# Kernel tuning notes

Measured on AMD Instinct MI355X. Metric: run time of the kernel, lower is better.

The kernel has to match this reference:

```python
import jax, jax.numpy as jnp
import numpy as np

B, S, D, NF = 4, 8192, 1024, 256

def setup_inputs() -> dict:
    key = jax.random.key(0)
    k1, k2, k3, k4 = jax.random.split(key, 4)
    x = jax.random.normal(k1, (B, S, D), dtype=jnp.float32)
    W_in = jax.random.normal(k2, (2 * NF, D), dtype=jnp.float32) * 0.02
    W_out = jax.random.normal(k3, (D, 2 * NF), dtype=jnp.float32) * 0.02
    log_decay = jnp.linspace(-3.0, -0.001, NF).astype(jnp.float32)
    frequencies = jax.random.normal(k4, (NF,), dtype=jnp.float32)
    return {"x": x, "W_in": W_in, "W_out": W_out,
            "log_decay": log_decay, "frequencies": frequencies}

def reference(x, W_in, W_out, log_decay, frequencies):
    b, s, d = x.shape
    nf = log_decay.shape[0]
    dt = jnp.float32(1.0)
    # system matrices
    decay = jax.nn.sigmoid(log_decay)                      # [nf]
    omega = frequencies * 0.1 * dt
    rot = jax.lax.complex(jnp.cos(omega), jnp.sin(omega))  # [nf] complex
    A = decay * rot                                        # [nf] complex
    # input projection -> complex signal u
    spectral = jnp.einsum('bsd,fd->bsf', x, W_in)          # [b,s,2nf]
    u = jax.lax.complex(spectral[..., :nf], spectral[..., nf:])  # [b,s,nf]
    # kernel: powers[t] = A^t via cumprod (matches torch numerics), times rot
    ones = jnp.ones((1, nf), dtype=A.dtype)
    A_rep = jnp.broadcast_to(A[None, :], (s - 1, nf))
    powers = jnp.cumprod(jnp.concatenate([ones, A_rep], axis=0), axis=0)  # [s,nf]
    kernel = powers * rot[None, :]                         # [s,nf]
    # FFT long convolution (zero-pad to 2s for linear conv)
    n_fft = 2 * s
    U_f = jnp.fft.fft(u, n=n_fft, axis=1)                  # [b,2s,nf]
    K_f = jnp.fft.fft(kernel, n=n_fft, axis=0)             # [2s,nf]
    y = jnp.fft.ifft(U_f * K_f[None, :, :], axis=1)[:, :s, :]  # [b,s,nf]
    feats = jnp.concatenate([y.real, y.imag], axis=-1)     # [b,s,2nf]
    return jnp.einsum('bsf,df->bsd', feats, W_out)         # [b,s,d]
```

## Files before the change

### kernel.cpp

```cpp
#include <hip/hip_runtime.h>
#include <math.h>
#include <stdint.h>

#define PB 4
#define PS 8192
#define PD 1024
#define PNF 256
#define PF2 512
#define PM 32768

#define CHUNK_L 32
#define WARM_W 32
#define NCHUNK (PS / CHUNK_L)

typedef __bf16 bf16x8 __attribute__((ext_vector_type(8)));
typedef float f32x4 __attribute__((ext_vector_type(4)));

__device__ __forceinline__ unsigned short f2bf(float f) {
  uint32_t b = __float_as_uint(f);
  b += 0x7FFFu + ((b >> 16) & 1u);
  return (unsigned short)(b >> 16);
}
__device__ __forceinline__ float bf2f(unsigned short u) {
  return __uint_as_float(((uint32_t)u) << 16);
}

__device__ __forceinline__ void gload16(const void* g, void* l) {
  __builtin_amdgcn_global_load_lds(
      (const __attribute__((address_space(1))) void*)g,
      (__attribute__((address_space(3))) void*)l, 16, 0, 0);
}

__global__ __launch_bounds__(256) void cvt_f32_bf16(
    const float* __restrict__ in, unsigned short* __restrict__ out, int n8) {
  int i = blockIdx.x * 256 + threadIdx.x;
  const int stride = gridDim.x * 256;
  for (; i < n8; i += stride) {
    const float4* p = (const float4*)(in + (size_t)i * 8);
    float4 a = p[0], b = p[1];
    float v[8] = {a.x, a.y, a.z, a.w, b.x, b.y, b.z, b.w};
    union { unsigned short u[8]; uint4 q; } o;
#pragma unroll
    for (int j = 0; j < 8; ++j) o.u[j] = f2bf(v[j]);
    *(uint4*)(out + (size_t)i * 8) = o.q;
  }
}

template <bool STORE_BF16>
__global__ __launch_bounds__(256, 2) void gemm_nt_mfma(
    const unsigned short* __restrict__ A, const unsigned short* __restrict__ Bt,
    void* __restrict__ Cv, int M, int N, int K) {
  __shared__ __align__(16) unsigned short As[128 * 32];
  __shared__ __align__(16) unsigned short Bs[128 * 32];
  const int tid = threadIdx.x;
  const int lane = tid & 63;
  const int w = tid >> 6;
  const int bm = blockIdx.y * 128;
  const int bn = blockIdx.x * 128;
  const int wm = (w >> 1) * 64;
  const int wn = (w & 1) * 64;

  const int lr = tid >> 2;
  const int lc = (tid & 3) * 8;
  const unsigned short* Ap = A + (size_t)(bm + lr) * K + lc;
  const unsigned short* Bp = Bt + (size_t)(bn + lr) * K + lc;
  char* AsB0 = (char*)As + (size_t)(w * 64) * 16;
  char* AsB1 = (char*)As + (size_t)(256 + w * 64) * 16;
  char* BsB0 = (char*)Bs + (size_t)(w * 64) * 16;
  char* BsB1 = (char*)Bs + (size_t)(256 + w * 64) * 16;

  const int fr = lane & 15;
  const int fk = (lane >> 4) * 8;

  f32x4 acc[4][4] = {};

  const int nk = K >> 5;
  for (int kk = 0; kk < nk; ++kk) {
    __syncthreads();
    gload16(Ap, AsB0);
    gload16(Ap + (size_t)64 * K, AsB1);
    gload16(Bp, BsB0);
    gload16(Bp + (size_t)64 * K, BsB1);
    Ap += 32; Bp += 32;
    __syncthreads();

    bf16x8 af[4], bfr[4];
#pragma unroll
    for (int mi = 0; mi < 4; ++mi)
      af[mi] = *(const bf16x8*)&As[(wm + mi * 16 + fr) * 32 + fk];
#pragma unroll
    for (int ni = 0; ni < 4; ++ni)
      bfr[ni] = *(const bf16x8*)&Bs[(wn + ni * 16 + fr) * 32 + fk];
#pragma unroll
    for (int mi = 0; mi < 4; ++mi)
#pragma unroll
      for (int ni = 0; ni < 4; ++ni)
        acc[mi][ni] = __builtin_amdgcn_mfma_f32_16x16x32_bf16(
            af[mi], bfr[ni], acc[mi][ni], 0, 0, 0);
  }

  const int orow0 = bm + wm + (lane >> 4) * 4;
  const int ocol0 = bn + wn + (lane & 15);
  if (STORE_BF16) {
    unsigned short* C = (unsigned short*)Cv;
#pragma unroll
    for (int mi = 0; mi < 4; ++mi)
#pragma unroll
      for (int ni = 0; ni < 4; ++ni) {
        const int col = ocol0 + ni * 16;
#pragma unroll
        for (int j = 0; j < 4; ++j) {
          const int row = orow0 + mi * 16 + j;
          C[(size_t)row * N + col] = f2bf(acc[mi][ni][j]);
        }
      }
  } else {
    float* C = (float*)Cv;
#pragma unroll
    for (int mi = 0; mi < 4; ++mi)
#pragma unroll
      for (int ni = 0; ni < 4; ++ni) {
        const int col = ocol0 + ni * 16;
#pragma unroll
        for (int j = 0; j < 4; ++j) {
          const int row = orow0 + mi * 16 + j;
          C[(size_t)row * N + col] = acc[mi][ni][j];
        }
      }
  }
}

__global__ __launch_bounds__(256) void scan_fused(
    const unsigned short* __restrict__ sp, const float* __restrict__ log_decay,
    const float* __restrict__ freq, unsigned short* __restrict__ feats) {
  const int tid = threadIdx.x;
  const int half = tid >> 7;
  const int fp = tid & 127;
  const int f0 = fp * 2;
  const int c = blockIdx.x * 2 + half;
  const int b = blockIdx.y;

  float Ar[2], Ai[2], rc_[2], rs_[2], hr[2] = {0.f, 0.f}, hi[2] = {0.f, 0.f};
#pragma unroll
  for (int k = 0; k < 2; ++k) {
    const float decay = 1.f / (1.f + expf(-log_decay[f0 + k]));
    const float om = freq[f0 + k] * 0.1f;
    rc_[k] = cosf(om); rs_[k] = sinf(om);
    Ar[k] = decay * rc_[k]; Ai[k] = decay * rs_[k];
  }

  const int t0 = c * CHUNK_L;
  int tw = t0 - WARM_W; if (tw < 0) tw = 0;
  const uint32_t* base = (const uint32_t*)(sp + (size_t)b * PS * PF2);
  uint32_t* ob = (uint32_t*)(feats + (size_t)b * PS * PF2);
  const int pr_off = f0 >> 1;
  const int pi_off = (PNF + f0) >> 1;

  for (int t = tw; t < t0; ++t) {
    const size_t rowu = (size_t)t * (PF2 / 2);
    uint32_t pr = base[rowu + pr_off];
    uint32_t pi = base[rowu + pi_off];
    float ur[2] = {bf2f((unsigned short)(pr & 0xffff)), bf2f((unsigned short)(pr >> 16))};
    float ui[2] = {bf2f((unsigned short)(pi & 0xffff)), bf2f((unsigned short)(pi >> 16))};
#pragma unroll
    for (int k = 0; k < 2; ++k) {
      float nr = fmaf(Ar[k], hr[k], fmaf(-Ai[k], hi[k], ur[k]));
      float ni = fmaf(Ar[k], hi[k], fmaf(Ai[k], hr[k], ui[k]));
      hr[k] = nr; hi[k] = ni;
    }
  }
  for (int t = t0; t < t0 + CHUNK_L; ++t) {
    const size_t rowu = (size_t)t * (PF2 / 2);
    uint32_t pr = base[rowu + pr_off];
    uint32_t pi = base[rowu + pi_off];
    float ur[2] = {bf2f((unsigned short)(pr & 0xffff)), bf2f((unsigned short)(pr >> 16))};
    float ui[2] = {bf2f((unsigned short)(pi & 0xffff)), bf2f((unsigned short)(pi >> 16))};
    uint32_t wr = 0, wi = 0;
#pragma unroll
    for (int k = 0; k < 2; ++k) {
      float nr = fmaf(Ar[k], hr[k], fmaf(-Ai[k], hi[k], ur[k]));
      float ni = fmaf(Ar[k], hi[k], fmaf(Ai[k], hr[k], ui[k]));
      hr[k] = nr; hi[k] = ni;
      const float yr = fmaf(rc_[k], hr[k], -rs_[k] * hi[k]);
      const float yi = fmaf(rc_[k], hi[k],  rs_[k] * hr[k]);
      wr |= (uint32_t)f2bf(yr) << (16 * k);
      wi |= (uint32_t)f2bf(yi) << (16 * k);
    }
    ob[rowu + pr_off] = wr;
    ob[rowu + pi_off] = wi;
  }
}

extern "C" void kernel_launch(void* const* d_in, const int* in_sizes, int n_in,
                              void* d_out, int out_size, void* d_ws, size_t ws_size,
                              hipStream_t stream) {
  const float* x         = (const float*)d_in[0];
  const float* W_in      = (const float*)d_in[1];
  const float* W_out     = (const float*)d_in[2];
  const float* log_decay = (const float*)d_in[3];
  const float* freq      = (const float*)d_in[4];
  float* out = (float*)d_out;

  unsigned short* xbf   = (unsigned short*)d_ws;
  unsigned short* wibf  = xbf + (size_t)PM * PD;
  unsigned short* wobf  = wibf + (size_t)PF2 * PD;
  unsigned short* spbf  = wobf + (size_t)PD * PF2;
  unsigned short* feats = xbf;

  cvt_f32_bf16<<<2048, 256, 0, stream>>>(x, xbf, PM * PD / 8);
  cvt_f32_bf16<<<256, 256, 0, stream>>>(W_in, wibf, PF2 * PD / 8);
  cvt_f32_bf16<<<256, 256, 0, stream>>>(W_out, wobf, PD * PF2 / 8);

  gemm_nt_mfma<true><<<dim3(PF2 / 128, PM / 128), 256, 0, stream>>>(
      xbf, wibf, spbf, PM, PF2, PD);

  scan_fused<<<dim3(NCHUNK / 2, PB), 256, 0, stream>>>(spbf, log_decay, freq, feats);

  gemm_nt_mfma<false><<<dim3(PD / 128, PM / 128), 256, 0, stream>>>(
      feats, wobf, out, PM, PD, PF2);
}
```

Measured before the change: 364.0 us.

## Replace GEMM with 256x256-tile 8-phase pipelined MFMA kernel

Replaces the simple 128x128 single-buffered GEMM with a 512-thread 256x256-tile kernel that double-buffers 64-wide K slices in 128 KB of dynamic LDS. It interleaves global-to-LDS loads with MFMA phases using explicit waitcnt, barriers and setprio, and applies an XOR swizzle to reduce LDS bank conflicts. It also pads the workspace buffers. The aim is to hide memory latency and raise MFMA utilisation. The cost is heavy LDS use (one block per CU) and fragile hand-tuned wait counts.

```diff
diff --git a/kernel.cpp b/kernel.cpp
--- a/kernel.cpp
+++ b/kernel.cpp
@@ -24,7 +24,6 @@
 __device__ __forceinline__ float bf2f(unsigned short u) {
   return __uint_as_float(((uint32_t)u) << 16);
 }
-
 __device__ __forceinline__ void gload16(const void* g, void* l) {
   __builtin_amdgcn_global_load_lds(
       (const __attribute__((address_space(1))) void*)g,
@@ -47,87 +46,116 @@
 }
 
 template <bool STORE_BF16>
-__global__ __launch_bounds__(256, 2) void gemm_nt_mfma(
-    const unsigned short* __restrict__ A, const unsigned short* __restrict__ Bt,
+__global__ __launch_bounds__(512, 2) void gemm_nt_8phase(
+    const unsigned short* __restrict__ Ag, const unsigned short* __restrict__ Bg,
     void* __restrict__ Cv, int M, int N, int K) {
-  __shared__ __align__(16) unsigned short As[128 * 32];
-  __shared__ __align__(16) unsigned short Bs[128 * 32];
+  extern __shared__ char smem[];
+  char* AtC = smem;
+  char* BtC = smem + 65536;
   const int tid = threadIdx.x;
   const int lane = tid & 63;
   const int w = tid >> 6;
-  const int bm = blockIdx.y * 128;
-  const int bn = blockIdx.x * 128;
-  const int wm = (w >> 1) * 64;
-  const int wn = (w & 1) * 64;
-
-  const int lr = tid >> 2;
-  const int lc = (tid & 3) * 8;
-  const unsigned short* Ap = A + (size_t)(bm + lr) * K + lc;
-  const unsigned short* Bp = Bt + (size_t)(bn + lr) * K + lc;
-  char* AsB0 = (char*)As + (size_t)(w * 64) * 16;
-  char* AsB1 = (char*)As + (size_t)(256 + w * 64) * 16;
-  char* BsB0 = (char*)Bs + (size_t)(w * 64) * 16;
-  char* BsB1 = (char*)Bs + (size_t)(256 + w * 64) * 16;
-
+  const int wr = w >> 2, wc = w & 3;
+  const int bm = blockIdx.y * 256, bn = blockIdx.x * 256;
   const int fr = lane & 15;
-  const int fk = (lane >> 4) * 8;
-
-  f32x4 acc[4][4] = {};
-
-  const int nk = K >> 5;
-  for (int kk = 0; kk < nk; ++kk) {
-    __syncthreads();
-    gload16(Ap, AsB0);
-    gload16(Ap + (size_t)64 * K, AsB1);
-    gload16(Bp, BsB0);
-    gload16(Bp + (size_t)64 * K, BsB1);
-    Ap += 32; Bp += 32;
-    __syncthreads();
-
-    bf16x8 af[4], bfr[4];
-#pragma unroll
-    for (int mi = 0; mi < 4; ++mi)
-      af[mi] = *(const bf16x8*)&As[(wm + mi * 16 + fr) * 32 + fk];
-#pragma unroll
-    for (int ni = 0; ni < 4; ++ni)
-      bfr[ni] = *(const bf16x8*)&Bs[(wn + ni * 16 + fr) * 32 + fk];
-#pragma unroll
-    for (int mi = 0; mi < 4; ++mi)
-#pragma unroll
-      for (int ni = 0; ni < 4; ++ni)
-        acc[mi][ni] = __builtin_amdgcn_mfma_f32_16x16x32_bf16(
-            af[mi], bfr[ni], acc[mi][ni], 0, 0, 0);
-  }
-
-  const int orow0 = bm + wm + (lane >> 4) * 4;
-  const int ocol0 = bn + wn + (lane & 15);
-  if (STORE_BF16) {
-    unsigned short* C = (unsigned short*)Cv;
-#pragma unroll
-    for (int mi = 0; mi < 4; ++mi)
-#pragma unroll
-      for (int ni = 0; ni < 4; ++ni) {
-        const int col = ocol0 + ni * 16;
-#pragma unroll
-        for (int j = 0; j < 4; ++j) {
-          const int row = orow0 + mi * 16 + j;
-          C[(size_t)row * N + col] = f2bf(acc[mi][ni][j]);
+  const int fkb = (lane >> 4) * 16;
+  const int sx = ((fr >> 2) & 1) << 5;
+  const int ko0 = fkb ^ sx;
+  const int ko1 = (64 + fkb) ^ sx;
+  const int srow = tid >> 3;
+  const int scol = ((tid & 7) * 8) ^ (((tid >> 5) & 1) << 4);
+  const unsigned short* Ab = Ag + (size_t)(bm + srow) * K + scol;
+  const unsigned short* Bb = Bg + (size_t)(bn + srow) * K + scol;
+  const int ldst = tid * 16;
+
+  f32x4 acc[2][2][4][2] = {};
+  bf16x8 af[4][2], bq[2][2];
+
+#define STG_A(kt, h, bs) { \
+    const unsigned short* g_ = Ab + (size_t)((h) * 128) * K + (kt) * 64; \
+    char* l_ = AtC + ((bs) << 15) + ((h) << 14) + ldst; \
+    gload16(g_, l_); gload16(g_ + (size_t)64 * K, l_ + 8192); }
+#define STG_B(kt, h, bs) { \
+    const unsigned short* g_ = Bb + (size_t)((h) * 128) * K + (kt) * 64; \
+    char* l_ = BtC + ((bs) << 15) + ((h) << 14) + ldst; \
+    gload16(g_, l_); gload16(g_ + (size_t)64 * K, l_ + 8192); }
+#define LDA(bs, QM) { _Pragma("unroll") for (int mi = 0; mi < 4; ++mi) { \
+    const char* p_ = AtC + ((bs) << 15) + (((QM) * 128 + wr * 64 + mi * 16 + fr) << 7); \
+    af[mi][0] = *(const bf16x8*)(p_ + ko0); af[mi][1] = *(const bf16x8*)(p_ + ko1); } }
+#define LDB(bs, QN) { _Pragma("unroll") for (int ni = 0; ni < 2; ++ni) { \
+    const char* p_ = BtC + ((bs) << 15) + (((QN) * 128 + wc * 32 + ni * 16 + fr) << 7); \
+    bq[ni][0] = *(const bf16x8*)(p_ + ko0); bq[ni][1] = *(const bf16x8*)(p_ + ko1); } }
+#define MM(QM, QN) { _Pragma("unroll") for (int mi = 0; mi < 4; ++mi) \
+    _Pragma("unroll") for (int ni = 0; ni < 2; ++ni) { \
+      acc[QM][QN][mi][ni] = __builtin_amdgcn_mfma_f32_16x16x32_bf16( \
+          af[mi][0], bq[ni][0], acc[QM][QN][mi][ni], 0, 0, 0); \
+      acc[QM][QN][mi][ni] = __builtin_amdgcn_mfma_f32_16x16x32_bf16( \
+          af[mi][1], bq[ni][1], acc[QM][QN][mi][ni], 0, 0, 0); } }
+#define BAR() __builtin_amdgcn_s_barrier()
+#define WL0() { asm volatile("s_waitcnt lgkmcnt(0)" ::: "memory"); \
+                __builtin_amdgcn_sched_barrier(0); }
+#define VM6() asm volatile("s_waitcnt vmcnt(6)" ::: "memory")
+#define P1() __builtin_amdgcn_s_setprio(1)
+#define P0() __builtin_amdgcn_s_setprio(0)
+
+  STG_A(0, 0, 0); STG_B(0, 1, 0); STG_A(0, 1, 0); STG_B(0, 0, 0);
+  STG_A(1, 0, 1); STG_B(1, 1, 1); STG_A(1, 1, 1);
+  VM6();
+  BAR();
+
+  const int iters = K >> 7;
+  for (int i = 0; i < iters; ++i) {
+    const int o1 = 2 * i + 1, e2 = 2 * i + 2, o3 = 2 * i + 3;
+    LDA(0, 0); LDB(0, 0); STG_B(o1, 0, 1);
+    BAR(); WL0(); P1(); MM(0, 0); P0(); BAR();
+    LDB(0, 1); STG_A(e2, 0, 0);
+    BAR(); WL0(); P1(); MM(0, 1); P0(); BAR();
+    LDA(0, 1); STG_B(e2, 1, 0);
+    BAR(); WL0(); P1(); MM(1, 1); P0(); BAR();
+    LDB(0, 0); STG_A(e2, 1, 0);
+    VM6();
+    BAR(); WL0(); P1(); MM(1, 0); P0(); BAR();
+    LDA(1, 0); LDB(1, 0); STG_B(e2, 0, 0);
+    BAR(); WL0(); P1(); MM(0, 0); P0(); BAR();
+    LDB(1, 1); STG_A(o3, 0, 1);
+    BAR(); WL0(); P1(); MM(0, 1); P0(); BAR();
+    LDA(1, 1); STG_B(o3, 1, 1);
+    BAR(); WL0(); P1(); MM(1, 1); P0(); BAR();
+    LDB(1, 0); STG_A(o3, 1, 1);
+    VM6();
+    BAR(); WL0(); P1(); MM(1, 0); P0(); BAR();
+  }
+
+  const int crow = bm + wr * 64 + (lane >> 4) * 4;
+  const int ccol = bn + wc * 32 + fr;
+#pragma unroll
+  for (int qm = 0; qm < 2; ++qm)
+#pragma unroll
+    for (int qn = 0; qn < 2; ++qn)
+#pragma unroll
+      for (int mi = 0; mi < 4; ++mi)
+#pragma unroll
+        for (int ni = 0; ni < 2; ++ni) {
+          const int col = ccol + qn * 128 + ni * 16;
+          if (STORE_BF16) {
+            unsigned short* C = (unsigned short*)Cv;
+#pragma unroll
+            for (int j = 0; j < 4; ++j)
+              C[(size_t)(crow + qm * 128 + mi * 16 + j) * N + col] =
+                  f2bf(acc[qm][qn][mi][ni][j]);
+          } else {
+            float* C = (float*)Cv;
+#pragma unroll
+            for (int j = 0; j < 4; ++j)
+              C[(size_t)(crow + qm * 128 + mi * 16 + j) * N + col] =
+                  acc[qm][qn][mi][ni][j];
+          }
         }
-      }
-  } else {
-    float* C = (float*)Cv;
-#pragma unroll
-    for (int mi = 0; mi < 4; ++mi)
-#pragma unroll
-      for (int ni = 0; ni < 4; ++ni) {
-        const int col = ocol0 + ni * 16;
-#pragma unroll
-        for (int j = 0; j < 4; ++j) {
-          const int row = orow0 + mi * 16 + j;
-          C[(size_t)row * N + col] = acc[mi][ni][j];
-        }
-      }
-  }
+#undef STG_A
+#undef STG_B
+#undef LDA
+#undef LDB
+#undef MM
 }
 
 __global__ __launch_bounds__(256) void scan_fused(
@@ -175,7 +203,7 @@
     uint32_t pi = base[rowu + pi_off];
     float ur[2] = {bf2f((unsigned short)(pr & 0xffff)), bf2f((unsigned short)(pr >> 16))};
     float ui[2] = {bf2f((unsigned short)(pi & 0xffff)), bf2f((unsigned short)(pi >> 16))};
-    uint32_t wr = 0, wi = 0;
+    uint32_t wr_ = 0, wi_ = 0;
 #pragma unroll
     for (int k = 0; k < 2; ++k) {
       float nr = fmaf(Ar[k], hr[k], fmaf(-Ai[k], hi[k], ur[k]));
@@ -183,11 +211,11 @@
       hr[k] = nr; hi[k] = ni;
       const float yr = fmaf(rc_[k], hr[k], -rs_[k] * hi[k]);
       const float yi = fmaf(rc_[k], hi[k],  rs_[k] * hr[k]);
-      wr |= (uint32_t)f2bf(yr) << (16 * k);
-      wi |= (uint32_t)f2bf(yi) << (16 * k);
+      wr_ |= (uint32_t)f2bf(yr) << (16 * k);
+      wi_ |= (uint32_t)f2bf(yi) << (16 * k);
     }
-    ob[rowu + pr_off] = wr;
-    ob[rowu + pi_off] = wi;
+    ob[rowu + pr_off] = wr_;
+    ob[rowu + pi_off] = wi_;
   }
 }
 
@@ -201,21 +229,21 @@
   const float* freq      = (const float*)d_in[4];
   float* out = (float*)d_out;
 
-  unsigned short* xbf   = (unsigned short*)d_ws;
-  unsigned short* wibf  = xbf + (size_t)PM * PD;
-  unsigned short* wobf  = wibf + (size_t)PF2 * PD;
-  unsigned short* spbf  = wobf + (size_t)PD * PF2;
+  unsigned short* xbf  = (unsigned short*)d_ws;
+  unsigned short* wibf = xbf + (size_t)PM * PD + 16384;
+  unsigned short* wobf = wibf + (size_t)PF2 * PD + 16384;
+  unsigned short* spbf = wobf + (size_t)PD * PF2 + 16384;
   unsigned short* feats = xbf;
 
   cvt_f32_bf16<<<2048, 256, 0, stream>>>(x, xbf, PM * PD / 8);
   cvt_f32_bf16<<<256, 256, 0, stream>>>(W_in, wibf, PF2 * PD / 8);
   cvt_f32_bf16<<<256, 256, 0, stream>>>(W_out, wobf, PD * PF2 / 8);
 
-  gemm_nt_mfma<true><<<dim3(PF2 / 128, PM / 128), 256, 0, stream>>>(
+  gemm_nt_8phase<true><<<dim3(PF2 / 256, PM / 256), 512, 131072, stream>>>(
       xbf, wibf, spbf, PM, PF2, PD);
 
   scan_fused<<<dim3(NCHUNK / 2, PB), 256, 0, stream>>>(spbf, log_decay, freq, feats);
 
-  gemm_nt_mfma<false><<<dim3(PD / 128, PM / 128), 256, 0, stream>>>(
+  gemm_nt_8phase<false><<<dim3(PD / 256, PM / 256), 512, 131072, stream>>>(
       feats, wobf, out, PM, PD, PF2);
 }
```

Measured after the change: 351.2 us. -3.5%, faster.
